# Kernel optimization log

Hardware: AMD Instinct MI355X
Metric: run time of the kernel (lower is better)

Reference implementation:

```python
import jax, jax.numpy as jnp
import numpy as np

N_EMBD = 768
N_HEAD = 12
HEAD_DIM = N_EMBD // N_HEAD
B = 4
L_MAIN = 1024
L_SIDE = 1024
HALF = L_SIDE // 2  # occurrences of each modality per row
LN_EPS = 1e-5


def setup_inputs() -> dict:
    key = jax.random.key(0)
    ks = jax.random.split(key, 16)
    x = jax.random.normal(ks[0], (B, L_MAIN, N_EMBD), jnp.float32)
    # ages in years, sorted per-row (events arrive in time order), all >= 0
    age = jnp.sort(jax.random.uniform(ks[1], (B, L_MAIN), jnp.float32) * 80.0, axis=1)
    mod_age = jnp.sort(jax.random.uniform(ks[2], (B, L_SIDE), jnp.float32) * 80.0, axis=1)
    # each row holds exactly HALF tokens of modality 2 and HALF of modality 3, randomly interleaved
    base = jnp.concatenate([jnp.full((HALF,), 2, jnp.int32), jnp.full((HALF,), 3, jnp.int32)])
    mod_idx = jax.vmap(lambda k: jax.random.permutation(k, base))(jax.random.split(ks[3], B))
    mod2_emb = jax.random.normal(ks[4], (B * HALF, N_EMBD), jnp.float32)
    mod3_emb = jax.random.normal(ks[5], (B * HALF, N_EMBD), jnp.float32)

    def lin(k, fan_out, fan_in):
        return 0.02 * jax.random.normal(k, (fan_out, fan_in), jnp.float32)

    params = dict(
        ln0_w=jnp.ones((N_EMBD,), jnp.float32), ln0_b=jnp.zeros((N_EMBD,), jnp.float32),
        ln1_w=jnp.ones((N_EMBD,), jnp.float32), ln1_b=jnp.zeros((N_EMBD,), jnp.float32),
        ln2_w=jnp.ones((N_EMBD,), jnp.float32), ln2_b=jnp.zeros((N_EMBD,), jnp.float32),
        q_w=lin(ks[6], N_EMBD, N_EMBD), q_b=jnp.zeros((N_EMBD,), jnp.float32),
        k_w=lin(ks[7], N_EMBD, N_EMBD), k_b=jnp.zeros((N_EMBD,), jnp.float32),
        v_w=lin(ks[8], N_EMBD, N_EMBD), v_b=jnp.zeros((N_EMBD,), jnp.float32),
        c_w=lin(ks[9], N_EMBD, N_EMBD), c_b=jnp.zeros((N_EMBD,), jnp.float32),
        fc_w=lin(ks[10], 4 * N_EMBD, N_EMBD), fc_b=jnp.zeros((4 * N_EMBD,), jnp.float32),
        proj_w=lin(ks[11], N_EMBD, 4 * N_EMBD), proj_b=jnp.zeros((N_EMBD,), jnp.float32),
    )
    return dict(x=x, age=age, mod_idx=mod_idx, mod_age=mod_age,
                mod2_emb=mod2_emb, mod3_emb=mod3_emb, **params)


def _ln(t, w, b):
    m = jnp.mean(t, axis=-1, keepdims=True)
    v = jnp.var(t, axis=-1, keepdims=True)
    return (t - m) * jax.lax.rsqrt(v + LN_EPS) * w + b


def _fuse_embed(mod_idx, mod_age, mod2_emb, mod3_emb):
    # torch: stable argsort by age, then scatter each modality's embeddings into
    # its matching positions in row-major nonzero order.
    order = jnp.argsort(mod_age, axis=1, stable=True)
    s_idx = jnp.take_along_axis(mod_idx, order, axis=1)  # [B, L_side]
    rows = jnp.arange(s_idx.shape[0])[:, None]
    def scatter_mod(val, m_emb):
        mask = s_idx == val
        occ = jnp.cumsum(mask, axis=1) - 1          # per-row occurrence counter
        gidx = rows * HALF + jnp.clip(occ, 0, HALF - 1)  # global row-major index
        return jnp.where(mask[..., None], m_emb[gidx], 0.0)
    return scatter_mod(2, mod2_emb) + scatter_mod(3, mod3_emb)


def _cross_fusion(x, age, mod_idx, mod_age, mod2_emb, mod3_emb,
                  ln0_w, ln0_b, ln1_w, ln1_b, ln2_w, ln2_b,
                  q_w, q_b, k_w, k_b, v_w, v_b, c_w, c_b,
                  fc_w, fc_b, proj_w, proj_b):
    mod_x = _fuse_embed(mod_idx, mod_age, mod2_emb, mod3_emb)  # [B, L_side, E]
    # time_attention_mask: query may attend to keys with key_age <= query_age, pad = key_age >= 0
    attn_mask = (age[:, :, None] >= mod_age[:, None, :]) & (mod_age >= 0.0)[:, None, :]
    attn_mask = attn_mask[:, None, :, :]  # [B, 1, L_main, L_side]

    xn = _ln(x, ln1_w, ln1_b)
    sn = _ln(mod_x, ln0_w, ln0_b)
    q = (xn @ q_w.T + q_b).reshape(B, L_MAIN, N_HEAD, HEAD_DIM).transpose(0, 2, 1, 3)
    k = (sn @ k_w.T + k_b).reshape(B, L_SIDE, N_HEAD, HEAD_DIM).transpose(0, 2, 1, 3)
    v = (sn @ v_w.T + v_b).reshape(B, L_SIDE, N_HEAD, HEAD_DIM).transpose(0, 2, 1, 3)

    att = jnp.einsum('bhqd,bhkd->bhqk', q, k) * (HEAD_DIM ** -0.5)
    all_masked = ~jnp.any(attn_mask, axis=-1, keepdims=True)
    # fully-masked rows: use 0 logits (uniform softmax) then zero out -> matches
    # torch's masked_fill(all_masked, 0) after nan softmax, but grad-safe.
    neg = jnp.where(all_masked, 0.0, -jnp.inf)
    att = jnp.where(attn_mask, att, neg)
    att = jax.nn.softmax(att, axis=-1)
    att = jnp.where(all_masked, 0.0, att)

    y = jnp.einsum('bhqk,bhkd->bhqd', att, v)
    y = y.transpose(0, 2, 1, 3).reshape(B, L_MAIN, N_EMBD)
    x = x + (y @ c_w.T + c_b)
    h = _ln(x, ln2_w, ln2_b)
    h = jax.nn.gelu(h @ fc_w.T + fc_b, approximate=False)
    x = x + (h @ proj_w.T + proj_b)
    return x


def reference(x, age, mod_idx, mod_age, mod2_emb, mod3_emb,
              ln0_w, ln0_b, ln1_w, ln1_b, ln2_w, ln2_b,
              q_w, q_b, k_w, k_b, v_w, v_b, c_w, c_b,
              fc_w, fc_b, proj_w, proj_b):
    return _cross_fusion(x, age, mod_idx, mod_age, mod2_emb, mod3_emb,
                         ln0_w, ln0_b, ln1_w, ln1_b, ln2_w, ln2_b,
                         q_w, q_b, k_w, k_b, v_w, v_b, c_w, c_b,
                         fc_w, fc_b, proj_w, proj_b)
```

## Files before the change

### kernel.cpp

```cpp
#include <hip/hip_runtime.h>

#define N_EMBD 768
#define SEQ    1024
#define NBATCH 4
#define NHEAD  12
#define HDIM   64
#define NROWS  4096
#define FFN    3072
#define W768   589824
#define WFC    2359296

typedef unsigned short u16;
typedef __bf16 bf16x8 __attribute__((ext_vector_type(8)));
typedef float  f32x4  __attribute__((ext_vector_type(4)));
typedef unsigned short u16x8 __attribute__((ext_vector_type(8)));

typedef const __attribute__((address_space(1))) unsigned int gu32;
typedef __attribute__((address_space(3))) unsigned int lu32;
#define GLL(g, l) __builtin_amdgcn_global_load_lds((gu32*)(g), (lu32*)(l), 16, 0, 0)

__device__ __forceinline__ u16 f2bf(float f) {
    union { float f; unsigned int i; } v; v.f = f;
    unsigned int r = v.i + 0x7fffu + ((v.i >> 16) & 1u);
    return (u16)(r >> 16);
}

__global__ __launch_bounds__(256) void cvt_weights(const float* __restrict__ qw,
                                                   const float* __restrict__ kw,
                                                   const float* __restrict__ vw,
                                                   const float* __restrict__ cw,
                                                   const float* __restrict__ fcw,
                                                   const float* __restrict__ pw,
                                                   u16* __restrict__ dst) {
    size_t e = ((size_t)blockIdx.x * 256 + threadIdx.x) * 4;
    const float* src; size_t base;
    if      (e < 1 * (size_t)W768) { src = qw;  base = 0; }
    else if (e < 2 * (size_t)W768) { src = kw;  base = 1 * (size_t)W768; }
    else if (e < 3 * (size_t)W768) { src = vw;  base = 2 * (size_t)W768; }
    else if (e < 4 * (size_t)W768) { src = cw;  base = 3 * (size_t)W768; }
    else if (e < 4 * (size_t)W768 + WFC) { src = fcw; base = 4 * (size_t)W768; }
    else { src = pw; base = 4 * (size_t)W768 + WFC; }
    float4 v = *(const float4*)(src + (e - base));
    ushort4 o;
    o.x = f2bf(v.x); o.y = f2bf(v.y); o.z = f2bf(v.z); o.w = f2bf(v.w);
    *(ushort4*)(dst + e) = o;
}

__global__ __launch_bounds__(1024) void prefix_kernel(const int* __restrict__ mod_idx,
                                                      int* __restrict__ g) {
    __shared__ int sc[1024];
    int b = blockIdx.x, j = threadIdx.x;
    int mi  = mod_idx[b * SEQ + j];
    int is2 = (mi == 2) ? 1 : 0;
    sc[j] = is2;
    __syncthreads();
    for (int off = 1; off < 1024; off <<= 1) {
        int add = (j >= off) ? sc[j - off] : 0;
        __syncthreads();
        sc[j] += add;
        __syncthreads();
    }
    int c2  = sc[j];
    int occ = is2 ? (c2 - 1) : (j - c2);
    occ = occ < 0 ? 0 : (occ > 511 ? 511 : occ);
    g[b * SEQ + j] = is2 ? (b * 512 + occ) : (2048 + b * 512 + occ);
}

__global__ __launch_bounds__(256) void ln_rows(const float* __restrict__ src,
                                               const float* __restrict__ src2,
                                               const int* __restrict__ g,
                                               const float* __restrict__ w,
                                               const float* __restrict__ b,
                                               u16* __restrict__ dst) {
    int row  = blockIdx.x * 4 + (threadIdx.x >> 6);
    int lane = threadIdx.x & 63;
    const float* p;
    if (g) {
        int gi = g[row];
        p = (gi < 2048) ? (src + (size_t)gi * N_EMBD)
                        : (src2 + (size_t)(gi - 2048) * N_EMBD);
    } else {
        p = src + (size_t)row * N_EMBD;
    }
    float vals[12];
    float s = 0.f, sq = 0.f;
#pragma unroll
    for (int c = 0; c < 12; c++) {
        float v = p[c * 64 + lane];
        vals[c] = v; s += v; sq += v * v;
    }
#pragma unroll
    for (int o = 32; o > 0; o >>= 1) { s += __shfl_xor(s, o); sq += __shfl_xor(sq, o); }
    float mean = s * (1.0f / 768.0f);
    float var  = sq * (1.0f / 768.0f) - mean * mean;
    float r    = rsqrtf(var + 1e-5f);
    u16* d = dst + (size_t)row * N_EMBD;
#pragma unroll
    for (int c = 0; c < 12; c++) {
        int idx = c * 64 + lane;
        d[idx] = f2bf((vals[c] - mean) * r * w[idx] + b[idx]);
    }
}


__device__ __forceinline__ void core128(const u16* __restrict__ A, const u16* __restrict__ W,
                                        int K, int m0, int n0, int t,
                                        u16* As, u16* Bs, f32x4 (&acc)[4][4]) {
    int w = t >> 6, lane = t & 63, quad = lane >> 4, l16 = lane & 15;
    int r16 = lane >> 2, c8 = (lane & 3) * 8;
    int wm = (w >> 1) * 64, wn = (w & 1) * 64;
    for (int k0 = 0; k0 < K; k0 += 32) {
        __syncthreads();
        const u16* ga = A + (size_t)(m0 + w * 32 + r16) * K + k0 + c8;
        const u16* gb = W + (size_t)(n0 + w * 32 + r16) * K + k0 + c8;
        GLL(ga,                  &As[(w * 32) * 32]);
        GLL(ga + 16 * (size_t)K, &As[(w * 32 + 16) * 32]);
        GLL(gb,                  &Bs[(w * 32) * 32]);
        GLL(gb + 16 * (size_t)K, &Bs[(w * 32 + 16) * 32]);
        __syncthreads();
        bf16x8 af[4], bfr[4];
#pragma unroll
        for (int i = 0; i < 4; i++)
            af[i] = *(const bf16x8*)&As[(wm + i * 16 + l16) * 32 + quad * 8];
#pragma unroll
        for (int j = 0; j < 4; j++)
            bfr[j] = *(const bf16x8*)&Bs[(wn + j * 16 + l16) * 32 + quad * 8];
#pragma unroll
        for (int i = 0; i < 4; i++)
#pragma unroll
            for (int j = 0; j < 4; j++)
                acc[i][j] = __builtin_amdgcn_mfma_f32_16x16x32_bf16(af[i], bfr[j], acc[i][j], 0, 0, 0);
    }
}

__device__ __forceinline__ void core64(const u16* __restrict__ A, const u16* __restrict__ W,
                                       int K, int kBeg, int kEnd, int m0, int n0, int t,
                                       u16* As, u16* Bs, f32x4 (&acc)[2][4]) {
    int w = t >> 6, lane = t & 63, quad = lane >> 4, l16 = lane & 15;
    int r16 = lane >> 2, c8 = (lane & 3) * 8;
    int wm = (w >> 1) * 32, wn = (w & 1) * 64;
    for (int k0 = kBeg; k0 < kEnd; k0 += 32) {
        __syncthreads();
        const u16* gb = W + (size_t)(n0 + w * 32 + r16) * K + k0 + c8;
        GLL(A + (size_t)(m0 + w * 16 + r16) * K + k0 + c8, &As[(w * 16) * 32]);
        GLL(gb,                  &Bs[(w * 32) * 32]);
        GLL(gb + 16 * (size_t)K, &Bs[(w * 32 + 16) * 32]);
        __syncthreads();
        bf16x8 af[2], bfr[4];
#pragma unroll
        for (int i = 0; i < 2; i++)
            af[i] = *(const bf16x8*)&As[(wm + i * 16 + l16) * 32 + quad * 8];
#pragma unroll
        for (int j = 0; j < 4; j++)
            bfr[j] = *(const bf16x8*)&Bs[(wn + j * 16 + l16) * 32 + quad * 8];
#pragma unroll
        for (int i = 0; i < 2; i++)
#pragma unroll
            for (int j = 0; j < 4; j++)
                acc[i][j] = __builtin_amdgcn_mfma_f32_16x16x32_bf16(af[i], bfr[j], acc[i][j], 0, 0, 0);
    }
}

__global__ __launch_bounds__(256) void gemm_qkv(const u16* __restrict__ xn,
                                                const u16* __restrict__ sn,
                                                const u16* __restrict__ wq,
                                                const float* __restrict__ qb,
                                                const float* __restrict__ kb,
                                                const float* __restrict__ vb,
                                                u16* __restrict__ outbase) {
    __shared__ u16 As[128 * 32], Bs[128 * 32];
    int z = blockIdx.z;
    const u16* A = (z == 0) ? xn : sn;
    const u16* W = wq + (size_t)z * W768;
    const float* bias = (z == 0) ? qb : ((z == 1) ? kb : vb);
    u16* C = outbase + (size_t)z * ((size_t)NROWS * N_EMBD);
    int m0 = blockIdx.y * 128, n0 = blockIdx.x * 128;
    int t = threadIdx.x;
    f32x4 acc[4][4];
#pragma unroll
    for (int i = 0; i < 4; i++)
#pragma unroll
        for (int j = 0; j < 4; j++) acc[i][j] = (f32x4){0.f, 0.f, 0.f, 0.f};
    core128(A, W, N_EMBD, m0, n0, t, As, Bs, acc);
    int w = t >> 6, lane = t & 63, quad = lane >> 4, l16 = lane & 15;
    int wm = (w >> 1) * 64, wn = (w & 1) * 64;
#pragma unroll
    for (int j = 0; j < 4; j++) {
        int col = n0 + wn + j * 16 + l16;
        float bv = bias[col];
#pragma unroll
        for (int i = 0; i < 4; i++) {
            int rowb = m0 + wm + i * 16 + quad * 4;
#pragma unroll
            for (int r = 0; r < 4; r++)
                C[(size_t)(rowb + r) * N_EMBD + col] = f2bf(acc[i][j][r] + bv);
        }
    }
}

__global__ __launch_bounds__(256) void gemm_fc(const u16* __restrict__ A,
                                               const u16* __restrict__ W,
                                               const float* __restrict__ bias,
                                               u16* __restrict__ C) {
    __shared__ u16 As[128 * 32], Bs[128 * 32];
    int m0 = blockIdx.y * 128, n0 = blockIdx.x * 128;
    int t = threadIdx.x;
    f32x4 acc[4][4];
#pragma unroll
    for (int i = 0; i < 4; i++)
#pragma unroll
        for (int j = 0; j < 4; j++) acc[i][j] = (f32x4){0.f, 0.f, 0.f, 0.f};
    core128(A, W, N_EMBD, m0, n0, t, As, Bs, acc);
    int w = t >> 6, lane = t & 63, quad = lane >> 4, l16 = lane & 15;
    int wm = (w >> 1) * 64, wn = (w & 1) * 64;
#pragma unroll
    for (int j = 0; j < 4; j++) {
        int col = n0 + wn + j * 16 + l16;
        float bv = bias[col];
#pragma unroll
        for (int i = 0; i < 4; i++) {
            int rowb = m0 + wm + i * 16 + quad * 4;
#pragma unroll
            for (int r = 0; r < 4; r++) {
                float v = acc[i][j][r] + bv;
                v = 0.5f * v * (1.0f + erff(v * 0.70710678118654752f));
                C[(size_t)(rowb + r) * FFN + col] = f2bf(v);
            }
        }
    }
}

__global__ __launch_bounds__(256) void gemm_cproj(const u16* __restrict__ A,
                                                  const u16* __restrict__ W,
                                                  const float* __restrict__ bias,
                                                  const float* __restrict__ Res,
                                                  float* __restrict__ C) {
    __shared__ u16 As[64 * 32], Bs[128 * 32];
    int m0 = blockIdx.y * 64, n0 = blockIdx.x * 128;
    int t = threadIdx.x;
    f32x4 acc[2][4];
#pragma unroll
    for (int i = 0; i < 2; i++)
#pragma unroll
        for (int j = 0; j < 4; j++) acc[i][j] = (f32x4){0.f, 0.f, 0.f, 0.f};
    core64(A, W, N_EMBD, 0, N_EMBD, m0, n0, t, As, Bs, acc);
    int w = t >> 6, lane = t & 63, quad = lane >> 4, l16 = lane & 15;
    int wm = (w >> 1) * 32, wn = (w & 1) * 64;
#pragma unroll
    for (int j = 0; j < 4; j++) {
        int col = n0 + wn + j * 16 + l16;
        float bv = bias[col];
#pragma unroll
        for (int i = 0; i < 2; i++) {
            int rowb = m0 + wm + i * 16 + quad * 4;
#pragma unroll
            for (int r = 0; r < 4; r++) {
                size_t idx = (size_t)(rowb + r) * N_EMBD + col;
                C[idx] = acc[i][j][r] + bv + Res[idx];
            }
        }
    }
}

__global__ __launch_bounds__(256) void gemm_proj_split(const u16* __restrict__ A,
                                                       const u16* __restrict__ W,
                                                       float* __restrict__ p0,
                                                       float* __restrict__ p1) {
    __shared__ u16 As[64 * 32], Bs[128 * 32];
    int z = blockIdx.z;
    float* P = z ? p1 : p0;
    int m0 = blockIdx.y * 64, n0 = blockIdx.x * 128;
    int t = threadIdx.x;
    f32x4 acc[2][4];
#pragma unroll
    for (int i = 0; i < 2; i++)
#pragma unroll
        for (int j = 0; j < 4; j++) acc[i][j] = (f32x4){0.f, 0.f, 0.f, 0.f};
    core64(A, W, FFN, z * (FFN / 2), (z + 1) * (FFN / 2), m0, n0, t, As, Bs, acc);
    int w = t >> 6, lane = t & 63, quad = lane >> 4, l16 = lane & 15;
    int wm = (w >> 1) * 32, wn = (w & 1) * 64;
#pragma unroll
    for (int j = 0; j < 4; j++) {
        int col = n0 + wn + j * 16 + l16;
#pragma unroll
        for (int i = 0; i < 2; i++) {
            int rowb = m0 + wm + i * 16 + quad * 4;
#pragma unroll
            for (int r = 0; r < 4; r++)
                P[(size_t)(rowb + r) * N_EMBD + col] = acc[i][j][r];
        }
    }
}

__global__ __launch_bounds__(256) void reduce_proj(const float* __restrict__ p0,
                                                   const float* __restrict__ p1,
                                                   const float* __restrict__ bias,
                                                   const float* __restrict__ x1,
                                                   float* __restrict__ out) {
    size_t idx = ((size_t)blockIdx.x * 256 + threadIdx.x) * 4;
    int col = (int)(idx % N_EMBD);
    float4 a = *(const float4*)(p0 + idx);
    float4 b = *(const float4*)(p1 + idx);
    float4 r = *(const float4*)(x1 + idx);
    float4 bb = *(const float4*)(bias + col);
    float4 o;
    o.x = a.x + b.x + r.x + bb.x;
    o.y = a.y + b.y + r.y + bb.y;
    o.z = a.z + b.z + r.z + bb.z;
    o.w = a.w + b.w + r.w + bb.w;
    *(float4*)(out + idx) = o;
}

#define KST 72

__global__ __launch_bounds__(256) void attn_kernel(const u16* __restrict__ Q,
                                                   const u16* __restrict__ K,
                                                   const u16* __restrict__ V,
                                                   const float* __restrict__ age,
                                                   const float* __restrict__ mod_age,
                                                   u16* __restrict__ Y) {
    __shared__ u16 Kl[64 * KST];
    __shared__ u16 Vt[64 * KST];
    __shared__ u16 Pl[4][16 * KST];
    __shared__ float mas[64];

    int bx = blockIdx.x;
    int qt = bx & 15;
    int bh = bx >> 4;
    int b = bh / NHEAD, h = bh % NHEAD;
    int t = threadIdx.x;
    int w = t >> 6, lane = t & 63, quad = lane >> 4, l16 = lane & 15;
    int q0 = qt * 64 + w * 16;

    size_t qrowbase = ((size_t)(b * SEQ + q0 + l16)) * N_EMBD + h * HDIM;
    bf16x8 qf0 = *(const bf16x8*)&Q[qrowbase + quad * 8];
    bf16x8 qf1 = *(const bf16x8*)&Q[qrowbase + 32 + quad * 8];

    float age_r[4];
#pragma unroll
    for (int r = 0; r < 4; r++) age_r[r] = age[b * SEQ + q0 + quad * 4 + r];
    float age_max_blk = age[b * SEQ + qt * 64 + 63];
    float mod_min     = mod_age[b * SEQ];

    float m_i[4] = {-1e30f, -1e30f, -1e30f, -1e30f};
    float l_i[4] = {0.f, 0.f, 0.f, 0.f};
    f32x4 o[4];
#pragma unroll
    for (int nt = 0; nt < 4; nt++) o[nt] = (f32x4){0.f, 0.f, 0.f, 0.f};

    for (int kt = 0; kt < 16; kt++) {
        if (mod_age[b * SEQ + kt * 64] > age_max_blk) break;
        __syncthreads();
#pragma unroll
        for (int i = 0; i < 2; i++) {
            int chunk = i * 256 + t;
            int krow = chunk >> 3, kc8 = chunk & 7;
            *(u16x8*)&Kl[krow * KST + kc8 * 8] =
                *(const u16x8*)(K + ((size_t)(b * SEQ + kt * 64 + krow)) * N_EMBD + h * HDIM + kc8 * 8);
            int vrow = chunk & 63, vc8 = chunk >> 6;
            u16x8 v8 = *(const u16x8*)(V + ((size_t)(b * SEQ + kt * 64 + vrow)) * N_EMBD + h * HDIM + vc8 * 8);
#pragma unroll
            for (int e = 0; e < 8; e++) Vt[(vc8 * 8 + e) * KST + vrow] = v8[e];
        }
        if (t < 64) mas[t] = mod_age[b * SEQ + kt * 64 + t];
        __syncthreads();

        float p[4][4];
#pragma unroll
        for (int jt = 0; jt < 4; jt++) {
            f32x4 s = (f32x4){0.f, 0.f, 0.f, 0.f};
            bf16x8 kf0 = *(const bf16x8*)&Kl[(jt * 16 + l16) * KST + quad * 8];
            bf16x8 kf1 = *(const bf16x8*)&Kl[(jt * 16 + l16) * KST + 32 + quad * 8];
            s = __builtin_amdgcn_mfma_f32_16x16x32_bf16(qf0, kf0, s, 0, 0, 0);
            s = __builtin_amdgcn_mfma_f32_16x16x32_bf16(qf1, kf1, s, 0, 0, 0);
            float mval = mas[jt * 16 + l16];
#pragma unroll
            for (int r = 0; r < 4; r++) {
                float sv = s[r] * 0.125f;
                p[jt][r] = (mval <= age_r[r]) ? sv : -1e30f;
            }
        }
        float alpha[4];
#pragma unroll
        for (int r = 0; r < 4; r++) {
            float mx = fmaxf(fmaxf(p[0][r], p[1][r]), fmaxf(p[2][r], p[3][r]));
#pragma unroll
            for (int msk = 1; msk < 16; msk <<= 1) mx = fmaxf(mx, __shfl_xor(mx, msk));
            float mnew = fmaxf(m_i[r], mx);
            alpha[r] = expf(m_i[r] - mnew);
            float srow = 0.f;
#pragma unroll
            for (int jt = 0; jt < 4; jt++) {
                float pv = expf(p[jt][r] - mnew);
                p[jt][r] = pv;
                srow += pv;
            }
#pragma unroll
            for (int msk = 1; msk < 16; msk <<= 1) srow += __shfl_xor(srow, msk);
            l_i[r] = l_i[r] * alpha[r] + srow;
            m_i[r] = mnew;
        }
#pragma unroll
        for (int jt = 0; jt < 4; jt++)
#pragma unroll
            for (int r = 0; r < 4; r++)
                Pl[w][(quad * 4 + r) * KST + jt * 16 + l16] = f2bf(p[jt][r]);
#pragma unroll
        for (int nt = 0; nt < 4; nt++)
#pragma unroll
            for (int r = 0; r < 4; r++) o[nt][r] *= alpha[r];
#pragma unroll
        for (int c = 0; c < 2; c++) {
            bf16x8 pf = *(const bf16x8*)&Pl[w][l16 * KST + c * 32 + quad * 8];
#pragma unroll
            for (int nt = 0; nt < 4; nt++) {
                bf16x8 vf = *(const bf16x8*)&Vt[(nt * 16 + l16) * KST + c * 32 + quad * 8];
                o[nt] = __builtin_amdgcn_mfma_f32_16x16x32_bf16(pf, vf, o[nt], 0, 0, 0);
            }
        }
    }
#pragma unroll
    for (int r = 0; r < 4; r++) {
        int qrow = q0 + quad * 4 + r;
        float inv = (age_r[r] >= mod_min) ? (1.0f / l_i[r]) : 0.0f;
#pragma unroll
        for (int nt = 0; nt < 4; nt++)
            Y[((size_t)(b * SEQ + qrow)) * N_EMBD + h * HDIM + nt * 16 + l16] =
                f2bf(o[nt][r] * inv);
    }
}

extern "C" void kernel_launch(void* const* d_in, const int* in_sizes, int n_in,
                              void* d_out, int out_size, void* d_ws, size_t ws_size,
                              hipStream_t stream) {
    const float* x       = (const float*)d_in[0];
    const float* age     = (const float*)d_in[1];
    const int*   mod_idx = (const int*)d_in[2];
    const float* mod_age = (const float*)d_in[3];
    const float* mod2    = (const float*)d_in[4];
    const float* mod3    = (const float*)d_in[5];
    const float* ln0w = (const float*)d_in[6],  *ln0b = (const float*)d_in[7];
    const float* ln1w = (const float*)d_in[8],  *ln1b = (const float*)d_in[9];
    const float* ln2w = (const float*)d_in[10], *ln2b = (const float*)d_in[11];
    const float* qb = (const float*)d_in[13];
    const float* kb = (const float*)d_in[15];
    const float* vb = (const float*)d_in[17];
    const float* cb = (const float*)d_in[19];
    const float* fcb = (const float*)d_in[21];
    const float* pb = (const float*)d_in[23];

    char* ws = (char*)d_ws;
    const size_t RB = (size_t)NROWS * N_EMBD * 2;
    int* g   = (int*)ws;
    u16* wq  = (u16*)(ws + 32768);
    u16* wc  = wq + 3 * (size_t)W768;
    u16* wfc = wq + 4 * (size_t)W768;
    u16* wp  = wq + 4 * (size_t)W768 + WFC;
    size_t off = 32768 + 2 * (4 * (size_t)W768 + 2 * (size_t)WFC);
    u16* xn   = (u16*)(ws + off); off += RB;
    u16* sn   = (u16*)(ws + off); off += RB;
    u16* qbuf = (u16*)(ws + off); off += RB;
    u16* kbuf = (u16*)(ws + off); off += RB;
    u16* vbuf = (u16*)(ws + off); off += RB;
    float* x1 = (float*)(ws + off); off += (size_t)NROWS * N_EMBD * 4;
    u16* hbuf = (u16*)(ws + off);
    u16* yb = xn;  u16* hn = qbuf;
    float* p0 = (float*)xn;
    float* p1 = (float*)kbuf;

    cvt_weights<<<(4 * W768 + 2 * WFC) / 1024, 256, 0, stream>>>(
        (const float*)d_in[12], (const float*)d_in[14], (const float*)d_in[16],
        (const float*)d_in[18], (const float*)d_in[20], (const float*)d_in[22], wq);
    prefix_kernel<<<NBATCH, 1024, 0, stream>>>(mod_idx, g);
    ln_rows<<<NROWS / 4, 256, 0, stream>>>(x, nullptr, nullptr, ln1w, ln1b, xn);
    ln_rows<<<NROWS / 4, 256, 0, stream>>>(mod2, mod3, g, ln0w, ln0b, sn);

    gemm_qkv<<<dim3(N_EMBD / 128, NROWS / 128, 3), 256, 0, stream>>>(xn, sn, wq, qb, kb, vb, qbuf);

    attn_kernel<<<NBATCH * NHEAD * 16, 256, 0, stream>>>(qbuf, kbuf, vbuf, age, mod_age, yb);

    gemm_cproj<<<dim3(N_EMBD / 128, NROWS / 64), 256, 0, stream>>>(yb, wc, cb, x, x1);
    ln_rows<<<NROWS / 4, 256, 0, stream>>>(x1, nullptr, nullptr, ln2w, ln2b, hn);
    gemm_fc<<<dim3(FFN / 128, NROWS / 128), 256, 0, stream>>>(hn, wfc, fcb, hbuf);
    gemm_proj_split<<<dim3(N_EMBD / 128, NROWS / 64, 2), 256, 0, stream>>>(hbuf, wp, p0, p1);
    reduce_proj<<<(NROWS * N_EMBD / 4) / 256, 256, 0, stream>>>(p0, p1, pb, x1, (float*)d_out);

    (void)in_sizes; (void)n_in; (void)out_size; (void)ws_size;
}
```

Baseline: 343.9 us.

## Prefetch K/V tiles into registers and reorder blocks heaviest-first in attention

The attention kernel now loads the next K/V tile and its mod_age values into registers while the current tile is being computed, which overlaps global-load latency with MFMA work. Block indices are remapped so that query tiles with the most key tiles run first. The number of key tiles is found up front with a ballot, mod_age values are passed through shuffles instead of LDS, masking is skipped for tiles that need none, and expf is replaced with __expf. These changes raise register pressure and trade a small amount of exp accuracy for speed.

```diff
diff --git a/kernel.cpp b/kernel.cpp
--- a/kernel.cpp
+++ b/kernel.cpp
@@ -102,7 +102,6 @@
     }
 }
 
-
 __device__ __forceinline__ void core128(const u16* __restrict__ A, const u16* __restrict__ W,
                                         int K, int m0, int n0, int t,
                                         u16* As, u16* Bs, f32x4 (&acc)[4][4]) {
@@ -322,11 +321,10 @@
     __shared__ u16 Kl[64 * KST];
     __shared__ u16 Vt[64 * KST];
     __shared__ u16 Pl[4][16 * KST];
-    __shared__ float mas[64];
 
     int bx = blockIdx.x;
-    int qt = bx & 15;
-    int bh = bx >> 4;
+    int qt = 15 - (bx / 48);
+    int bh = bx % 48;
     int b = bh / NHEAD, h = bh % NHEAD;
     int t = threadIdx.x;
     int w = t >> 6, lane = t & 63, quad = lane >> 4, l16 = lane & 15;
@@ -339,8 +337,18 @@
     float age_r[4];
 #pragma unroll
     for (int r = 0; r < 4; r++) age_r[r] = age[b * SEQ + q0 + quad * 4 + r];
+    float age_q0      = __shfl(age_r[0], 0);
     float age_max_blk = age[b * SEQ + qt * 64 + 63];
     float mod_min     = mod_age[b * SEQ];
+
+    float mv0 = (lane < 16) ? mod_age[b * SEQ + lane * 64] : 1e30f;
+    unsigned long long bm = __ballot(mv0 > age_max_blk);
+    int nkt = bm ? (__ffsll(bm) - 1) : 16;
+
+    int krow0 = t >> 3,        kc8 = (t & 7) * 8;
+    int krow1 = 32 + (t >> 3);
+    int vrow  = t & 63;
+    int vc8_0 = t >> 6, vc8_1 = 4 + (t >> 6);
 
     float m_i[4] = {-1e30f, -1e30f, -1e30f, -1e30f};
     float l_i[4] = {0.f, 0.f, 0.f, 0.f};
@@ -348,23 +356,39 @@
 #pragma unroll
     for (int nt = 0; nt < 4; nt++) o[nt] = (f32x4){0.f, 0.f, 0.f, 0.f};
 
-    for (int kt = 0; kt < 16; kt++) {
-        if (mod_age[b * SEQ + kt * 64] > age_max_blk) break;
-        __syncthreads();
-#pragma unroll
-        for (int i = 0; i < 2; i++) {
-            int chunk = i * 256 + t;
-            int krow = chunk >> 3, kc8 = chunk & 7;
-            *(u16x8*)&Kl[krow * KST + kc8 * 8] =
-                *(const u16x8*)(K + ((size_t)(b * SEQ + kt * 64 + krow)) * N_EMBD + h * HDIM + kc8 * 8);
-            int vrow = chunk & 63, vc8 = chunk >> 6;
-            u16x8 v8 = *(const u16x8*)(V + ((size_t)(b * SEQ + kt * 64 + vrow)) * N_EMBD + h * HDIM + vc8 * 8);
-#pragma unroll
-            for (int e = 0; e < 8; e++) Vt[(vc8 * 8 + e) * KST + vrow] = v8[e];
-        }
-        if (t < 64) mas[t] = mod_age[b * SEQ + kt * 64 + t];
-        __syncthreads();
-
+    u16x8 kr0, kr1, vr0, vr1;
+    float mreg = 0.f;
+    if (nkt > 0) {
+        size_t kb = ((size_t)(b * SEQ)) * N_EMBD + h * HDIM;
+        kr0 = *(const u16x8*)(K + kb + (size_t)krow0 * N_EMBD + kc8);
+        kr1 = *(const u16x8*)(K + kb + (size_t)krow1 * N_EMBD + kc8);
+        vr0 = *(const u16x8*)(V + kb + (size_t)vrow * N_EMBD + vc8_0 * 8);
+        vr1 = *(const u16x8*)(V + kb + (size_t)vrow * N_EMBD + vc8_1 * 8);
+        mreg = mod_age[b * SEQ + lane];
+    }
+
+    for (int kt = 0; kt < nkt; kt++) {
+        __syncthreads();
+        *(u16x8*)&Kl[krow0 * KST + kc8] = kr0;
+        *(u16x8*)&Kl[krow1 * KST + kc8] = kr1;
+#pragma unroll
+        for (int e = 0; e < 8; e++) Vt[(vc8_0 * 8 + e) * KST + vrow] = vr0[e];
+#pragma unroll
+        for (int e = 0; e < 8; e++) Vt[(vc8_1 * 8 + e) * KST + vrow] = vr1[e];
+        float mcur = mreg;
+        __syncthreads();
+
+        if (kt + 1 < nkt) {
+            size_t kb = ((size_t)(b * SEQ + (kt + 1) * 64)) * N_EMBD + h * HDIM;
+            kr0 = *(const u16x8*)(K + kb + (size_t)krow0 * N_EMBD + kc8);
+            kr1 = *(const u16x8*)(K + kb + (size_t)krow1 * N_EMBD + kc8);
+            vr0 = *(const u16x8*)(V + kb + (size_t)vrow * N_EMBD + vc8_0 * 8);
+            vr1 = *(const u16x8*)(V + kb + (size_t)vrow * N_EMBD + vc8_1 * 8);
+            mreg = mod_age[b * SEQ + (kt + 1) * 64 + lane];
+        }
+
+        float tile_max = __shfl(mcur, 63);
+        bool need_mask = tile_max > age_q0;
         float p[4][4];
 #pragma unroll
         for (int jt = 0; jt < 4; jt++) {
@@ -373,11 +397,11 @@
             bf16x8 kf1 = *(const bf16x8*)&Kl[(jt * 16 + l16) * KST + 32 + quad * 8];
             s = __builtin_amdgcn_mfma_f32_16x16x32_bf16(qf0, kf0, s, 0, 0, 0);
             s = __builtin_amdgcn_mfma_f32_16x16x32_bf16(qf1, kf1, s, 0, 0, 0);
-            float mval = mas[jt * 16 + l16];
+            float mval = __shfl(mcur, jt * 16 + l16);
 #pragma unroll
             for (int r = 0; r < 4; r++) {
                 float sv = s[r] * 0.125f;
-                p[jt][r] = (mval <= age_r[r]) ? sv : -1e30f;
+                p[jt][r] = (!need_mask || mval <= age_r[r]) ? sv : -1e30f;
             }
         }
         float alpha[4];
@@ -387,11 +411,11 @@
 #pragma unroll
             for (int msk = 1; msk < 16; msk <<= 1) mx = fmaxf(mx, __shfl_xor(mx, msk));
             float mnew = fmaxf(m_i[r], mx);
-            alpha[r] = expf(m_i[r] - mnew);
+            alpha[r] = __expf(m_i[r] - mnew);
             float srow = 0.f;
 #pragma unroll
             for (int jt = 0; jt < 4; jt++) {
-                float pv = expf(p[jt][r] - mnew);
+                float pv = __expf(p[jt][r] - mnew);
                 p[jt][r] = pv;
                 srow += pv;
             }
```

Measured after the change: 314.1 us. 1.1x faster.
